# Kernel tuning notes

Hardware: AMD Instinct MI355X
Metric: run time of the kernel (lower is better)

## Reference

```python
import jax, jax.numpy as jnp
import numpy as np

B, S, D, H = 2, 2048, 1024, 16
DH = D // H  # head_dim = 64


def setup_inputs() -> dict:
    key = jax.random.key(0)
    ks = jax.random.split(key, 10)
    inp = {
        "query": jax.random.normal(ks[0], (B, S, D), jnp.float32),
        "key": jax.random.normal(ks[1], (B, S, D), jnp.float32),
        "value": jax.random.normal(ks[2], (B, S, D), jnp.float32),
        "mask": jnp.ones((B, S), jnp.int32),
        # per-head q/k/v projections stacked over the head axis [H, D, DH]
        "Wq": jax.random.normal(ks[3], (H, D, DH), jnp.float32) * 0.02,
        "bq": jnp.zeros((H, DH), jnp.float32),
        "Wk": jax.random.normal(ks[4], (H, D, DH), jnp.float32) * 0.02,
        "bk": jnp.zeros((H, DH), jnp.float32),
        "Wv": jax.random.normal(ks[5], (H, D, DH), jnp.float32) * 0.02,
        "bv": jnp.zeros((H, DH), jnp.float32),
        # output projection fc: Linear(D, D)
        "Wo": jax.random.normal(ks[6], (D, D), jnp.float32) * 0.02,
        "bo": jnp.zeros((D,), jnp.float32),
    }
    return inp


def reference(query, key, value, mask, Wq, bq, Wk, bk, Wv, bv, Wo, bo):
    scale = 1.0 / jnp.sqrt(jnp.asarray(DH, query.dtype))
    # batched per-head projections: [B,S,D] x [H,D,DH] -> [B,H,S,DH]
    q = jnp.einsum('bsd,hde->bhse', query, Wq) + bq[None, :, None, :]
    k = jnp.einsum('bsd,hde->bhse', key, Wk) + bk[None, :, None, :]
    v = jnp.einsum('bsd,hde->bhse', value, Wv) + bv[None, :, None, :]
    # scaled dot-product attention scores [B,H,Sq,Sk]
    scores = jnp.einsum('bhqe,bhke->bhqk', q, k) * scale
    scores = jnp.where(mask[:, None, None, :] == 0, jnp.asarray(-1e9, scores.dtype), scores)
    attn = jax.nn.softmax(scores, axis=-1)
    ctx = jnp.einsum('bhqk,bhke->bhqe', attn, v)          # [B,H,S,DH]
    ctx = ctx.transpose(0, 2, 1, 3).reshape(query.shape[0], -1, H * DH)  # concat heads
    return ctx @ Wo + bo
```

## Files before the change

kernel.cpp:

```cpp
#include <hip/hip_runtime.h>
#include <stdint.h>
#include <math.h>


typedef __attribute__((ext_vector_type(8))) short short8;
typedef __attribute__((ext_vector_type(4))) float floatx4;

#define LOG2E 1.44269504088896340736f

__device__ __forceinline__ unsigned short f32_bf16(float f) {
  union { float f; unsigned u; } c; c.f = f;
  return (unsigned short)((c.u + 0x7FFFu + ((c.u >> 16) & 1u)) >> 16);
}
__device__ __forceinline__ float bf16_f32(unsigned short u) {
  union { unsigned u; float f; } c; c.u = ((unsigned)u) << 16;
  return c.f;
}
__device__ __forceinline__ void gld16(const void* g, void* l) {
  __builtin_amdgcn_global_load_lds((const __attribute__((address_space(1))) void*)g,
                                   (__attribute__((address_space(3))) void*)l, 16, 0, 0);
}


__global__ __launch_bounds__(256) void prep_kernel(
    const float* __restrict__ qf, const float* __restrict__ kf, const float* __restrict__ vf,
    const float* __restrict__ w0, const float* __restrict__ w1, const float* __restrict__ w2,
    const float* __restrict__ wo, const int* __restrict__ mask,
    unsigned short* __restrict__ oq, unsigned short* __restrict__ ok, unsigned short* __restrict__ ov,
    unsigned short* __restrict__ o0, unsigned short* __restrict__ o1, unsigned short* __restrict__ o2,
    unsigned short* __restrict__ oo, float* __restrict__ mb) {
  __shared__ float t[32][33];
  const int y = blockIdx.y, bx = blockIdx.x;
  if (y < 3) {
    if (y == 0 && bx < 16) {
      int j = bx * 256 + threadIdx.x;
      mb[j] = (mask[j] == 0) ? (-1.0e9f * LOG2E) : 0.0f;
    }
    const float* in = (y == 0) ? qf : (y == 1) ? kf : vf;
    unsigned short* out = (y == 0) ? oq : (y == 1) ? ok : ov;
    int i = bx * 256 + threadIdx.x;
    float4 v = reinterpret_cast<const float4*>(in)[i];
    ushort4 o;
    o.x = f32_bf16(v.x); o.y = f32_bf16(v.y); o.z = f32_bf16(v.z); o.w = f32_bf16(v.w);
    reinterpret_cast<ushort4*>(out)[i] = o;
    return;
  }
  const int tx = threadIdx.x & 31, ty = threadIdx.x >> 5;
  const float* in; unsigned short* out; int R, C, z, r0, c0;
  if (bx < 3072) {
    const int zb = bx >> 6, rem = bx & 63;
    const int sel = zb >> 4; z = zb & 15;
    in = (sel == 0) ? w0 : (sel == 1) ? w1 : w2;
    out = (sel == 0) ? o0 : (sel == 1) ? o1 : o2;
    R = 1024; C = 64; r0 = (rem >> 1) * 32; c0 = (rem & 1) * 32;
  } else {
    const int t2 = bx - 3072;
    in = wo; out = oo; R = 1024; C = 1024; z = 0;
    r0 = (t2 >> 5) * 32; c0 = (t2 & 31) * 32;
  }
  const float* inp = in + (size_t)z * R * C;
  #pragma unroll
  for (int j = 0; j < 4; ++j)
    t[ty + j * 8][tx] = inp[(size_t)(r0 + ty + j * 8) * C + c0 + tx];
  __syncthreads();
  #pragma unroll
  for (int j = 0; j < 4; ++j)
    out[((size_t)z * C + c0 + ty + j * 8) * R + r0 + tx] = f32_bf16(t[tx][ty + j * 8]);
}


__global__ __launch_bounds__(512, 2) void gemm_proj_kernel(
    const unsigned short* __restrict__ qin, const unsigned short* __restrict__ kin,
    const unsigned short* __restrict__ vin,
    const unsigned short* __restrict__ WqT, const unsigned short* __restrict__ WkT,
    const unsigned short* __restrict__ WvT,
    const float* __restrict__ bq, const float* __restrict__ bk, const float* __restrict__ bv,
    unsigned short* __restrict__ Qp, unsigned short* __restrict__ Kp,
    unsigned short* __restrict__ Vt) {
  __shared__ unsigned short As[2][2][128 * 64];
  __shared__ unsigned short Bs[2][2][128 * 64];

  const int z = blockIdx.y;
  const int x = blockIdx.x;
  const int r = x & 7, q = x >> 3;
  int mt, nt;
  if (z < 2) { mt = r * 2 + (q >> 2); nt = q & 3; }
  else       { nt = r * 2 + (q >> 2); mt = q & 3; }
  const int blockM = mt * 256, blockN = nt * 256;

  const unsigned short* A  = (z == 0) ? qin : (z == 1) ? kin : WvT;
  const unsigned short* Bt = (z == 0) ? WqT : (z == 1) ? WkT : vin;
  const float* bias = (z == 0) ? bq : (z == 1) ? bk : bv;

  const int tid = threadIdx.x;
  const int w = tid >> 6, lane = tid & 63;
  const int quad = lane >> 4, l15 = lane & 15;
  const int wm = w & 1, wn = w >> 1;

  const int lr8 = lane >> 3;
  const int lc8 = lane & 7;
  const int gcs = lc8 ^ lr8;

  auto stage = [&](int k0, int buf) {
    #pragma unroll
    for (int h = 0; h < 2; ++h)
      #pragma unroll
      for (int s2 = 0; s2 < 2; ++s2) {
        const int rl = s2 * 64 + w * 8;
        gld16(A + (size_t)(blockM + h * 128 + rl + lr8) * 1024 + k0 + gcs * 8,
              &As[buf][h][rl * 64]);
      }
    #pragma unroll
    for (int h = 0; h < 2; ++h)
      #pragma unroll
      for (int s2 = 0; s2 < 2; ++s2) {
        const int rl = s2 * 64 + w * 8;
        gld16(Bt + (size_t)(blockN + h * 128 + rl + lr8) * 1024 + k0 + gcs * 8,
              &Bs[buf][h][rl * 64]);
      }
  };

  floatx4 acc[8][4];
  #pragma unroll
  for (int mi = 0; mi < 8; ++mi)
    #pragma unroll
    for (int ni = 0; ni < 4; ++ni)
      acc[mi][ni] = (floatx4){0.f, 0.f, 0.f, 0.f};

  stage(0, 0);
  __syncthreads();

  const int brb = (wn & 1) * 64;

  for (int st = 0; st < 16; ++st) {
    const int buf = st & 1;
    const unsigned short* Ah = &As[buf][wm][0];
    const unsigned short* Bh = &Bs[buf][wn >> 1][0];
    short8 af[4][2], b0[2][2], b1[2][2];

    if (st + 1 < 16) stage((st + 1) * 64, buf ^ 1);
    #pragma unroll
    for (int mi = 0; mi < 4; ++mi) {
      const int row = mi * 16 + l15;
      #pragma unroll
      for (int kk = 0; kk < 2; ++kk)
        af[mi][kk] = *(const short8*)(Ah + row * 64 + (((kk * 4 + quad) ^ (row & 7)) << 3));
    }
    #pragma unroll
    for (int ni = 0; ni < 2; ++ni) {
      const int row = brb + ni * 16 + l15;
      #pragma unroll
      for (int kk = 0; kk < 2; ++kk)
        b0[ni][kk] = *(const short8*)(Bh + row * 64 + (((kk * 4 + quad) ^ (row & 7)) << 3));
    }
    __builtin_amdgcn_s_barrier();
    __builtin_amdgcn_s_setprio(1);
    #pragma unroll
    for (int mi = 0; mi < 4; ++mi)
      #pragma unroll
      for (int ni = 0; ni < 2; ++ni)
        #pragma unroll
        for (int kk = 0; kk < 2; ++kk)
          acc[mi][ni] = __builtin_amdgcn_mfma_f32_16x16x32_bf16(af[mi][kk], b0[ni][kk], acc[mi][ni], 0, 0, 0);
    __builtin_amdgcn_s_setprio(0);
    __builtin_amdgcn_s_barrier();

    #pragma unroll
    for (int ni = 0; ni < 2; ++ni) {
      const int row = brb + (ni + 2) * 16 + l15;
      #pragma unroll
      for (int kk = 0; kk < 2; ++kk)
        b1[ni][kk] = *(const short8*)(Bh + row * 64 + (((kk * 4 + quad) ^ (row & 7)) << 3));
    }
    __builtin_amdgcn_s_barrier();
    __builtin_amdgcn_s_setprio(1);
    #pragma unroll
    for (int mi = 0; mi < 4; ++mi)
      #pragma unroll
      for (int ni = 0; ni < 2; ++ni)
        #pragma unroll
        for (int kk = 0; kk < 2; ++kk)
          acc[mi][ni + 2] = __builtin_amdgcn_mfma_f32_16x16x32_bf16(af[mi][kk], b1[ni][kk], acc[mi][ni + 2], 0, 0, 0);
    __builtin_amdgcn_s_setprio(0);
    __builtin_amdgcn_s_barrier();

    #pragma unroll
    for (int mi = 0; mi < 4; ++mi) {
      const int row = (mi + 4) * 16 + l15;
      #pragma unroll
      for (int kk = 0; kk < 2; ++kk)
        af[mi][kk] = *(const short8*)(Ah + row * 64 + (((kk * 4 + quad) ^ (row & 7)) << 3));
    }
    __builtin_amdgcn_s_barrier();
    __builtin_amdgcn_s_setprio(1);
    #pragma unroll
    for (int mi = 0; mi < 4; ++mi)
      #pragma unroll
      for (int ni = 0; ni < 2; ++ni)
        #pragma unroll
        for (int kk = 0; kk < 2; ++kk)
          acc[mi + 4][ni + 2] = __builtin_amdgcn_mfma_f32_16x16x32_bf16(af[mi][kk], b1[ni][kk], acc[mi + 4][ni + 2], 0, 0, 0);
    __builtin_amdgcn_s_setprio(0);
    __builtin_amdgcn_s_barrier();

    __builtin_amdgcn_s_setprio(1);
    #pragma unroll
    for (int mi = 0; mi < 4; ++mi)
      #pragma unroll
      for (int ni = 0; ni < 2; ++ni)
        #pragma unroll
        for (int kk = 0; kk < 2; ++kk)
          acc[mi + 4][ni] = __builtin_amdgcn_mfma_f32_16x16x32_bf16(af[mi][kk], b0[ni][kk], acc[mi + 4][ni], 0, 0, 0);
    __builtin_amdgcn_s_setprio(0);
    __syncthreads();
  }

  unsigned short* Cw = (w < 4) ? ((unsigned short*)As + w * 8192)
                               : ((unsigned short*)Bs + (w - 4) * 8192);
  const int pc = lc8 ^ lr8;

  if (z < 2) {
    unsigned short* outp = z ? Kp : Qp;
    const int n0 = blockN + wn * 64;
    const int m0 = blockM + wm * 128;
    float bn[4];
    #pragma unroll
    for (int ni = 0; ni < 4; ++ni) bn[ni] = bias[n0 + ni * 16 + l15];
    #pragma unroll
    for (int mi = 0; mi < 8; ++mi)
      #pragma unroll
      for (int ni = 0; ni < 4; ++ni)
        #pragma unroll
        for (int rr = 0; rr < 4; ++rr) {
          const int row = mi * 16 + quad * 4 + rr;
          const int col = ni * 16 + l15;
          Cw[row * 64 + (((col >> 3) ^ (row & 7)) << 3) + (col & 7)] =
              f32_bf16(acc[mi][ni][rr] + bn[ni]);
        }
    const size_t bb = (size_t)(m0 >> 11);
    const int h = n0 >> 6, s0 = m0 & 2047;
    unsigned short* dst = outp + ((bb * 16 + h) * 2048 + s0) * 64;
    #pragma unroll
    for (int ps = 0; ps < 16; ++ps) {
      const int lr = ps * 8 + lr8;
      *(short8*)(dst + lr * 64 + lc8 * 8) = *(const short8*)(Cw + lr * 64 + pc * 8);
    }
  } else {
    const int m0 = blockM + wm * 128;
    const int n0 = blockN + wn * 64;
    #pragma unroll
    for (int mi = 0; mi < 8; ++mi) {
      float bm[4];
      #pragma unroll
      for (int rr = 0; rr < 4; ++rr) bm[rr] = bias[m0 + mi * 16 + quad * 4 + rr];
      #pragma unroll
      for (int ni = 0; ni < 4; ++ni)
        #pragma unroll
        for (int rr = 0; rr < 4; ++rr) {
          const int row = mi * 16 + quad * 4 + rr;
          const int col = ni * 16 + l15;
          Cw[row * 64 + (((col >> 3) ^ (row & 7)) << 3) + (col & 7)] =
              f32_bf16(acc[mi][ni][rr] + bm[rr]);
        }
    }
    const size_t bb = (size_t)(n0 >> 11);
    const int s0 = n0 & 2047;
    unsigned short* dst = Vt + (bb * 1024 + m0) * 2048 + s0;
    #pragma unroll
    for (int ps = 0; ps < 16; ++ps) {
      const int lr = ps * 8 + lr8;
      *(short8*)(dst + (size_t)lr * 2048 + lc8 * 8) = *(const short8*)(Cw + lr * 64 + pc * 8);
    }
  }
}


__global__ __launch_bounds__(256) void gemm_out_kernel(
    const unsigned short* __restrict__ A, const unsigned short* __restrict__ Bt,
    const float* __restrict__ bias, float* __restrict__ out, int K, int N) {
  __shared__ unsigned short As[2][128 * 64];
  __shared__ unsigned short Bs[2][64 * 64];
  const int tid = threadIdx.x;
  const int w = tid >> 6, lane = tid & 63;
  const int quad = lane >> 4, l15 = lane & 15;
  const int wm = w & 1, wn = w >> 1;
  const int lr8 = lane >> 3, lc8 = lane & 7;
  const int gcs = lc8 ^ lr8;
  const int l = blockIdx.x, r = l & 7, j = l >> 3;
  const int blockM = (r * 4 + (j & 3)) * 128;
  const int blockN = (j >> 2) * 64;

  floatx4 acc[4][2];
  #pragma unroll
  for (int mi = 0; mi < 4; ++mi)
    #pragma unroll
    for (int ni = 0; ni < 2; ++ni)
      acc[mi][ni] = (floatx4){0.f, 0.f, 0.f, 0.f};

  auto stage = [&](int k0, int buf) {
    #pragma unroll
    for (int i = 0; i < 4; ++i) {
      const int rl = w * 32 + i * 8;
      gld16(A + (size_t)(blockM + rl + lr8) * K + k0 + gcs * 8, As[buf] + rl * 64);
    }
    #pragma unroll
    for (int i = 0; i < 2; ++i) {
      const int rl = w * 16 + i * 8;
      gld16(Bt + (size_t)(blockN + rl + lr8) * K + k0 + gcs * 8, Bs[buf] + rl * 64);
    }
  };

  const int iters = K >> 6;
  stage(0, 0);
  for (int it = 0; it < iters; ++it) {
    __syncthreads();
    if (it + 1 < iters) stage((it + 1) * 64, (it + 1) & 1);
    const unsigned short* Asb = As[it & 1];
    const unsigned short* Bsb = Bs[it & 1];
    short8 bf[2][2];
    #pragma unroll
    for (int ni = 0; ni < 2; ++ni) {
      const int row = wn * 32 + ni * 16 + l15;
      #pragma unroll
      for (int kk = 0; kk < 2; ++kk)
        bf[ni][kk] = *(const short8*)(Bsb + row * 64 + (((kk * 4 + quad) ^ (row & 7)) << 3));
    }
    #pragma unroll
    for (int mi = 0; mi < 4; ++mi) {
      const int row = wm * 64 + mi * 16 + l15;
      #pragma unroll
      for (int kk = 0; kk < 2; ++kk) {
        short8 af = *(const short8*)(Asb + row * 64 + (((kk * 4 + quad) ^ (row & 7)) << 3));
        #pragma unroll
        for (int ni = 0; ni < 2; ++ni)
          acc[mi][ni] = __builtin_amdgcn_mfma_f32_16x16x32_bf16(af, bf[ni][kk], acc[mi][ni], 0, 0, 0);
      }
    }
  }

  #pragma unroll
  for (int mi = 0; mi < 4; ++mi)
    #pragma unroll
    for (int ni = 0; ni < 2; ++ni) {
      const int n = blockN + wn * 32 + ni * 16 + l15;
      const float bv = bias[n];
      #pragma unroll
      for (int rr = 0; rr < 4; ++rr) {
        const int m = blockM + wm * 64 + mi * 16 + quad * 4 + rr;
        out[(size_t)m * N + n] = acc[mi][ni][rr] + bv;
      }
    }
}


__global__ __launch_bounds__(256) void attn_kernel(
    const unsigned short* __restrict__ Q, const unsigned short* __restrict__ Kg,
    const unsigned short* __restrict__ Vt, const float* __restrict__ maskAdd,
    unsigned short* __restrict__ ctx) {
  const int S = 2048;
  const int tid = threadIdx.x;
  const int w = tid >> 6, lane = tid & 63, quad = lane >> 4, l15 = lane & 15;
  const int l = blockIdx.x, r8 = l & 7, j8 = l >> 3;
  const int bh = r8 * 4 + (j8 & 3);
  const int qb = j8 >> 2;
  const int b = bh >> 4, h = bh & 15;
  const int q0 = qb * 128;

  __shared__ unsigned short Ks[2][128 * 64];
  __shared__ unsigned short Vs[2][64 * 128];
  __shared__ unsigned short Ps[4][32 * 64];
  unsigned short* Pw = Ps[w];

  const unsigned short* Qb = Q + (size_t)bh * S * 64;
  const unsigned short* Kb = Kg + (size_t)bh * S * 64;
  const unsigned short* Vb = Vt + (size_t)bh * 64 * S;
  const float* mb = maskAdd + (size_t)b * S;

  const float qs = 0.125f * LOG2E;
  short8 qf[2][2];
  #pragma unroll
  for (int mi = 0; mi < 2; ++mi)
    #pragma unroll
    for (int kq = 0; kq < 2; ++kq) {
      short8 v = *(const short8*)(Qb + (size_t)(q0 + w * 32 + mi * 16 + l15) * 64 + kq * 32 + quad * 8);
      #pragma unroll
      for (int jj = 0; jj < 8; ++jj)
        v[jj] = (short)f32_bf16(bf16_f32((unsigned short)v[jj]) * qs);
      qf[mi][kq] = v;
    }

  short8 onesf;
  #pragma unroll
  for (int jj = 0; jj < 8; ++jj) onesf[jj] = (short)0x3F80;

  floatx4 O[2][4], ls[2];
  #pragma unroll
  for (int mi = 0; mi < 2; ++mi) {
    #pragma unroll
    for (int ne = 0; ne < 4; ++ne) O[mi][ne] = (floatx4){0.f, 0.f, 0.f, 0.f};
    ls[mi] = (floatx4){0.f, 0.f, 0.f, 0.f};
  }

  auto stage_kv = [&](int t, int buf) {
    const int kv0 = t * 128;
    #pragma unroll
    for (int i = 0; i < 4; ++i) {
      int r0 = w * 32 + i * 8;
      int row = r0 + (lane >> 3);
      int cg = (lane & 7) ^ (row & 7);
      gld16(Kb + (size_t)(kv0 + row) * 64 + cg * 8, Ks[buf] + r0 * 64);
    }
    #pragma unroll
    for (int i = 0; i < 4; ++i) {
      int r0 = w * 16 + i * 4;
      int row = r0 + (lane >> 4);
      int p = lane & 15;
      int cg = (p & 8) | ((p & 7) ^ (row & 7));
      gld16(Vb + (size_t)row * S + kv0 + cg * 8, Vs[buf] + r0 * 128);
    }
  };

  stage_kv(0, 0);
  for (int t = 0; t < 16; ++t) {
    const int kv0 = t * 128;
    __syncthreads();
    float ma[8];
    #pragma unroll
    for (int ni = 0; ni < 8; ++ni) ma[ni] = mb[kv0 + ni * 16 + l15];
    if (t + 1 < 16) stage_kv(t + 1, (t + 1) & 1);
    const unsigned short* Ksb = Ks[t & 1];
    const unsigned short* Vsb = Vs[t & 1];

    #pragma unroll
    for (int ph = 0; ph < 2; ++ph) {
      floatx4 sc[2][4];
      #pragma unroll
      for (int ni = 0; ni < 4; ++ni) {
        const int key = (ph * 4 + ni) * 16 + l15;
        short8 kf0 = *(const short8*)(Ksb + key * 64 + ((quad) ^ (l15 & 7)) * 8);
        short8 kf1 = *(const short8*)(Ksb + key * 64 + ((4 + quad) ^ (l15 & 7)) * 8);
        #pragma unroll
        for (int mi = 0; mi < 2; ++mi) {
          floatx4 s = (floatx4){0.f, 0.f, 0.f, 0.f};
          s = __builtin_amdgcn_mfma_f32_16x16x32_bf16(qf[mi][0], kf0, s, 0, 0, 0);
          s = __builtin_amdgcn_mfma_f32_16x16x32_bf16(qf[mi][1], kf1, s, 0, 0, 0);
          sc[mi][ni] = s;
        }
      }
      #pragma unroll
      for (int mi = 0; mi < 2; ++mi)
        #pragma unroll
        for (int rr = 0; rr < 4; ++rr) {
          const int row = mi * 16 + quad * 4 + rr;
          const int g = (row + (row >> 3)) & 7;
          #pragma unroll
          for (int ni = 0; ni < 4; ++ni) {
            float p = __builtin_amdgcn_exp2f(sc[mi][ni][rr] + ma[ph * 4 + ni]);
            union { float f; unsigned u; } c; c.f = p;
            const int ch = (ni * 2 + (l15 >> 3)) ^ g;
            Pw[row * 64 + (ch & 7) * 8 + (l15 & 7)] = (unsigned short)(c.u >> 16);
          }
        }
      #pragma unroll
      for (int kkl = 0; kkl < 2; ++kkl) {
        const int kk = ph * 2 + kkl;
        short8 pfr[2], vfr[4];
        #pragma unroll
        for (int mi = 0; mi < 2; ++mi) {
          const int gp = (2 * mi + l15 + (l15 >> 3)) & 7;
          pfr[mi] = *(const short8*)(Pw + (mi * 16 + l15) * 64 + ((kkl * 4 + quad) ^ gp) * 8);
        }
        #pragma unroll
        for (int ne = 0; ne < 4; ++ne) {
          const int c = kk * 4 + quad;
          vfr[ne] = *(const short8*)(Vsb + (ne * 16 + l15) * 128 + ((c & 8) | ((c & 7) ^ (l15 & 7))) * 8);
        }
        #pragma unroll
        for (int mi = 0; mi < 2; ++mi) {
          #pragma unroll
          for (int ne = 0; ne < 4; ++ne)
            O[mi][ne] = __builtin_amdgcn_mfma_f32_16x16x32_bf16(pfr[mi], vfr[ne], O[mi][ne], 0, 0, 0);
          ls[mi] = __builtin_amdgcn_mfma_f32_16x16x32_bf16(pfr[mi], onesf, ls[mi], 0, 0, 0);
        }
      }
    }
  }

  #pragma unroll
  for (int mi = 0; mi < 2; ++mi)
    #pragma unroll
    for (int rr = 0; rr < 4; ++rr) {
      const float inv = __builtin_amdgcn_rcpf(ls[mi][rr]);
      const int s = q0 + w * 32 + mi * 16 + quad * 4 + rr;
      #pragma unroll
      for (int ne = 0; ne < 4; ++ne)
        ctx[((size_t)b * S + s) * 1024 + h * 64 + ne * 16 + l15] = f32_bf16(O[mi][ne][rr] * inv);
    }
}


extern "C" void kernel_launch(void* const* d_in, const int* in_sizes, int n_in,
                              void* d_out, int out_size, void* d_ws, size_t ws_size,
                              hipStream_t stream) {
  const float* query = (const float*)d_in[0];
  const float* key   = (const float*)d_in[1];
  const float* value = (const float*)d_in[2];
  const int*   mask  = (const int*)d_in[3];
  const float* Wq = (const float*)d_in[4];
  const float* bq = (const float*)d_in[5];
  const float* Wk = (const float*)d_in[6];
  const float* bk = (const float*)d_in[7];
  const float* Wv = (const float*)d_in[8];
  const float* bv = (const float*)d_in[9];
  const float* Wo = (const float*)d_in[10];
  const float* bo = (const float*)d_in[11];
  float* out = (float*)d_out;

  char* ws = (char*)d_ws;
  const size_t MB = 1024 * 1024;
  unsigned short* qin  = (unsigned short*)(ws + 0);
  unsigned short* kin  = (unsigned short*)(ws + 8 * MB);
  unsigned short* vin  = (unsigned short*)(ws + 16 * MB);
  unsigned short* WqT  = (unsigned short*)(ws + 24 * MB);
  unsigned short* WkT  = (unsigned short*)(ws + 26 * MB);
  unsigned short* WvT  = (unsigned short*)(ws + 28 * MB);
  unsigned short* WoT  = (unsigned short*)(ws + 30 * MB);
  unsigned short* Qp   = (unsigned short*)(ws + 32 * MB);
  unsigned short* Kp   = (unsigned short*)(ws + 40 * MB);
  unsigned short* Vt   = (unsigned short*)(ws + 48 * MB);
  float* maskAdd       = (float*)(ws + 56 * MB);
  unsigned short* ctxb = qin;

  prep_kernel<<<dim3(4096, 4), 256, 0, stream>>>(query, key, value, Wq, Wk, Wv, Wo, mask,
                                                 qin, kin, vin, WqT, WkT, WvT, WoT, maskAdd);
  gemm_proj_kernel<<<dim3(64, 3), 512, 0, stream>>>(qin, kin, vin, WqT, WkT, WvT,
                                                    bq, bk, bv, Qp, Kp, Vt);
  attn_kernel<<<dim3(512), 256, 0, stream>>>(Qp, Kp, Vt, maskAdd, ctxb);
  gemm_out_kernel<<<dim3(512), 256, 0, stream>>>(ctxb, WoT, bo, out, 1024, 1024);
}
```

Baseline: 229.4 us.

## Shrink projection GEMM tiles to 128x128 with 256 threads and simpler pipeline

The QKV projection GEMM moves from 256x256 tiles with 512 threads to 128x128 tiles with 256 threads, so the grid grows from 192 to 768 blocks. This is meant to fill the GPU's compute units better, since 192 blocks underfill a 256-CU device. The interleaved barrier and setprio MFMA schedule is replaced with a plain double-buffered loop. In exchange each block reuses less data per load, raising global and LDS traffic per FLOP, and loses the fine-grained load/compute interleaving.

```diff
diff --git a/kernel.cpp b/kernel.cpp
--- a/kernel.cpp
+++ b/kernel.cpp
@@ -69,7 +69,7 @@
 }
 
 
-__global__ __launch_bounds__(512, 2) void gemm_proj_kernel(
+__global__ __launch_bounds__(256) void gemm_proj_kernel(
     const unsigned short* __restrict__ qin, const unsigned short* __restrict__ kin,
     const unsigned short* __restrict__ vin,
     const unsigned short* __restrict__ WqT, const unsigned short* __restrict__ WkT,
@@ -77,16 +77,15 @@
     const float* __restrict__ bq, const float* __restrict__ bk, const float* __restrict__ bv,
     unsigned short* __restrict__ Qp, unsigned short* __restrict__ Kp,
     unsigned short* __restrict__ Vt) {
-  __shared__ unsigned short As[2][2][128 * 64];
-  __shared__ unsigned short Bs[2][2][128 * 64];
-
-  const int z = blockIdx.y;
-  const int x = blockIdx.x;
-  const int r = x & 7, q = x >> 3;
+  __shared__ unsigned short As[2][128 * 64];
+  __shared__ unsigned short Bs[2][128 * 64];
+
+  const int z = blockIdx.y, bx = blockIdx.x;
+  const int r = bx & 7, j = bx >> 3;
   int mt, nt;
-  if (z < 2) { mt = r * 2 + (q >> 2); nt = q & 3; }
-  else       { nt = r * 2 + (q >> 2); mt = q & 3; }
-  const int blockM = mt * 256, blockN = nt * 256;
+  if (z < 2) { mt = r * 4 + (j & 3); nt = j >> 2; }
+  else       { nt = r * 4 + (j & 3); mt = j >> 2; }
+  const int blockM = mt * 128, blockN = nt * 128;
 
   const unsigned short* A  = (z == 0) ? qin : (z == 1) ? kin : WvT;
   const unsigned short* Bt = (z == 0) ? WqT : (z == 1) ? WkT : vin;
@@ -96,138 +95,69 @@
   const int w = tid >> 6, lane = tid & 63;
   const int quad = lane >> 4, l15 = lane & 15;
   const int wm = w & 1, wn = w >> 1;
-
-  const int lr8 = lane >> 3;
-  const int lc8 = lane & 7;
+  const int lr8 = lane >> 3, lc8 = lane & 7;
   const int gcs = lc8 ^ lr8;
 
   auto stage = [&](int k0, int buf) {
     #pragma unroll
-    for (int h = 0; h < 2; ++h)
-      #pragma unroll
-      for (int s2 = 0; s2 < 2; ++s2) {
-        const int rl = s2 * 64 + w * 8;
-        gld16(A + (size_t)(blockM + h * 128 + rl + lr8) * 1024 + k0 + gcs * 8,
-              &As[buf][h][rl * 64]);
-      }
-    #pragma unroll
-    for (int h = 0; h < 2; ++h)
-      #pragma unroll
-      for (int s2 = 0; s2 < 2; ++s2) {
-        const int rl = s2 * 64 + w * 8;
-        gld16(Bt + (size_t)(blockN + h * 128 + rl + lr8) * 1024 + k0 + gcs * 8,
-              &Bs[buf][h][rl * 64]);
-      }
+    for (int i = 0; i < 4; ++i) {
+      const int rl = w * 32 + i * 8;
+      gld16(A + (size_t)(blockM + rl + lr8) * 1024 + k0 + gcs * 8, As[buf] + rl * 64);
+    }
+    #pragma unroll
+    for (int i = 0; i < 4; ++i) {
+      const int rl = w * 32 + i * 8;
+      gld16(Bt + (size_t)(blockN + rl + lr8) * 1024 + k0 + gcs * 8, Bs[buf] + rl * 64);
+    }
   };
 
-  floatx4 acc[8][4];
-  #pragma unroll
-  for (int mi = 0; mi < 8; ++mi)
+  floatx4 acc[4][4];
+  #pragma unroll
+  for (int mi = 0; mi < 4; ++mi)
     #pragma unroll
     for (int ni = 0; ni < 4; ++ni)
       acc[mi][ni] = (floatx4){0.f, 0.f, 0.f, 0.f};
 
   stage(0, 0);
+  for (int it = 0; it < 16; ++it) {
+    __syncthreads();
+    if (it + 1 < 16) stage((it + 1) * 64, (it + 1) & 1);
+    const unsigned short* Asb = As[it & 1];
+    const unsigned short* Bsb = Bs[it & 1];
+    short8 bf[4][2];
+    #pragma unroll
+    for (int ni = 0; ni < 4; ++ni) {
+      const int row = wn * 64 + ni * 16 + l15;
+      #pragma unroll
+      for (int kk = 0; kk < 2; ++kk)
+        bf[ni][kk] = *(const short8*)(Bsb + row * 64 + (((kk * 4 + quad) ^ (row & 7)) << 3));
+    }
+    #pragma unroll
+    for (int mi = 0; mi < 4; ++mi) {
+      const int row = wm * 64 + mi * 16 + l15;
+      #pragma unroll
+      for (int kk = 0; kk < 2; ++kk) {
+        short8 af = *(const short8*)(Asb + row * 64 + (((kk * 4 + quad) ^ (row & 7)) << 3));
+        #pragma unroll
+        for (int ni = 0; ni < 4; ++ni)
+          acc[mi][ni] = __builtin_amdgcn_mfma_f32_16x16x32_bf16(af, bf[ni][kk], acc[mi][ni], 0, 0, 0);
+      }
+    }
+  }
   __syncthreads();
 
-  const int brb = (wn & 1) * 64;
-
-  for (int st = 0; st < 16; ++st) {
-    const int buf = st & 1;
-    const unsigned short* Ah = &As[buf][wm][0];
-    const unsigned short* Bh = &Bs[buf][wn >> 1][0];
-    short8 af[4][2], b0[2][2], b1[2][2];
-
-    if (st + 1 < 16) stage((st + 1) * 64, buf ^ 1);
-    #pragma unroll
-    for (int mi = 0; mi < 4; ++mi) {
-      const int row = mi * 16 + l15;
-      #pragma unroll
-      for (int kk = 0; kk < 2; ++kk)
-        af[mi][kk] = *(const short8*)(Ah + row * 64 + (((kk * 4 + quad) ^ (row & 7)) << 3));
-    }
-    #pragma unroll
-    for (int ni = 0; ni < 2; ++ni) {
-      const int row = brb + ni * 16 + l15;
-      #pragma unroll
-      for (int kk = 0; kk < 2; ++kk)
-        b0[ni][kk] = *(const short8*)(Bh + row * 64 + (((kk * 4 + quad) ^ (row & 7)) << 3));
-    }
-    __builtin_amdgcn_s_barrier();
-    __builtin_amdgcn_s_setprio(1);
-    #pragma unroll
-    for (int mi = 0; mi < 4; ++mi)
-      #pragma unroll
-      for (int ni = 0; ni < 2; ++ni)
-        #pragma unroll
-        for (int kk = 0; kk < 2; ++kk)
-          acc[mi][ni] = __builtin_amdgcn_mfma_f32_16x16x32_bf16(af[mi][kk], b0[ni][kk], acc[mi][ni], 0, 0, 0);
-    __builtin_amdgcn_s_setprio(0);
-    __builtin_amdgcn_s_barrier();
-
-    #pragma unroll
-    for (int ni = 0; ni < 2; ++ni) {
-      const int row = brb + (ni + 2) * 16 + l15;
-      #pragma unroll
-      for (int kk = 0; kk < 2; ++kk)
-        b1[ni][kk] = *(const short8*)(Bh + row * 64 + (((kk * 4 + quad) ^ (row & 7)) << 3));
-    }
-    __builtin_amdgcn_s_barrier();
-    __builtin_amdgcn_s_setprio(1);
-    #pragma unroll
-    for (int mi = 0; mi < 4; ++mi)
-      #pragma unroll
-      for (int ni = 0; ni < 2; ++ni)
-        #pragma unroll
-        for (int kk = 0; kk < 2; ++kk)
-          acc[mi][ni + 2] = __builtin_amdgcn_mfma_f32_16x16x32_bf16(af[mi][kk], b1[ni][kk], acc[mi][ni + 2], 0, 0, 0);
-    __builtin_amdgcn_s_setprio(0);
-    __builtin_amdgcn_s_barrier();
-
-    #pragma unroll
-    for (int mi = 0; mi < 4; ++mi) {
-      const int row = (mi + 4) * 16 + l15;
-      #pragma unroll
-      for (int kk = 0; kk < 2; ++kk)
-        af[mi][kk] = *(const short8*)(Ah + row * 64 + (((kk * 4 + quad) ^ (row & 7)) << 3));
-    }
-    __builtin_amdgcn_s_barrier();
-    __builtin_amdgcn_s_setprio(1);
-    #pragma unroll
-    for (int mi = 0; mi < 4; ++mi)
-      #pragma unroll
-      for (int ni = 0; ni < 2; ++ni)
-        #pragma unroll
-        for (int kk = 0; kk < 2; ++kk)
-          acc[mi + 4][ni + 2] = __builtin_amdgcn_mfma_f32_16x16x32_bf16(af[mi][kk], b1[ni][kk], acc[mi + 4][ni + 2], 0, 0, 0);
-    __builtin_amdgcn_s_setprio(0);
-    __builtin_amdgcn_s_barrier();
-
-    __builtin_amdgcn_s_setprio(1);
-    #pragma unroll
-    for (int mi = 0; mi < 4; ++mi)
-      #pragma unroll
-      for (int ni = 0; ni < 2; ++ni)
-        #pragma unroll
-        for (int kk = 0; kk < 2; ++kk)
-          acc[mi + 4][ni] = __builtin_amdgcn_mfma_f32_16x16x32_bf16(af[mi][kk], b0[ni][kk], acc[mi + 4][ni], 0, 0, 0);
-    __builtin_amdgcn_s_setprio(0);
-    __syncthreads();
-  }
-
-  unsigned short* Cw = (w < 4) ? ((unsigned short*)As + w * 8192)
-                               : ((unsigned short*)Bs + (w - 4) * 8192);
+  unsigned short* Cw = (unsigned short*)As + w * 4096;
   const int pc = lc8 ^ lr8;
 
   if (z < 2) {
     unsigned short* outp = z ? Kp : Qp;
     const int n0 = blockN + wn * 64;
-    const int m0 = blockM + wm * 128;
+    const int m0 = blockM + wm * 64;
     float bn[4];
     #pragma unroll
     for (int ni = 0; ni < 4; ++ni) bn[ni] = bias[n0 + ni * 16 + l15];
     #pragma unroll
-    for (int mi = 0; mi < 8; ++mi)
+    for (int mi = 0; mi < 4; ++mi)
       #pragma unroll
       for (int ni = 0; ni < 4; ++ni)
         #pragma unroll
@@ -241,15 +171,15 @@
     const int h = n0 >> 6, s0 = m0 & 2047;
     unsigned short* dst = outp + ((bb * 16 + h) * 2048 + s0) * 64;
     #pragma unroll
-    for (int ps = 0; ps < 16; ++ps) {
+    for (int ps = 0; ps < 8; ++ps) {
       const int lr = ps * 8 + lr8;
       *(short8*)(dst + lr * 64 + lc8 * 8) = *(const short8*)(Cw + lr * 64 + pc * 8);
     }
   } else {
-    const int m0 = blockM + wm * 128;
+    const int m0 = blockM + wm * 64;
     const int n0 = blockN + wn * 64;
     #pragma unroll
-    for (int mi = 0; mi < 8; ++mi) {
+    for (int mi = 0; mi < 4; ++mi) {
       float bm[4];
       #pragma unroll
       for (int rr = 0; rr < 4; ++rr) bm[rr] = bias[m0 + mi * 16 + quad * 4 + rr];
@@ -267,7 +197,7 @@
     const int s0 = n0 & 2047;
     unsigned short* dst = Vt + (bb * 1024 + m0) * 2048 + s0;
     #pragma unroll
-    for (int ps = 0; ps < 16; ++ps) {
+    for (int ps = 0; ps < 8; ++ps) {
       const int lr = ps * 8 + lr8;
       *(short8*)(dst + (size_t)lr * 2048 + lc8 * 8) = *(const short8*)(Cw + lr * 64 + pc * 8);
     }
@@ -533,8 +463,8 @@
 
   prep_kernel<<<dim3(4096, 4), 256, 0, stream>>>(query, key, value, Wq, Wk, Wv, Wo, mask,
                                                  qin, kin, vin, WqT, WkT, WvT, WoT, maskAdd);
-  gemm_proj_kernel<<<dim3(64, 3), 512, 0, stream>>>(qin, kin, vin, WqT, WkT, WvT,
-                                                    bq, bk, bv, Qp, Kp, Vt);
+  gemm_proj_kernel<<<dim3(256, 3), 256, 0, stream>>>(qin, kin, vin, WqT, WkT, WvT,
+                                                     bq, bk, bv, Qp, Kp, Vt);
   attn_kernel<<<dim3(512), 256, 0, stream>>>(Qp, Kp, Vt, maskAdd, ctxb);
   gemm_out_kernel<<<dim3(512), 256, 0, stream>>>(ctxb, WoT, bo, out, 1024, 1024);
 }
```

New measurement: 237.1 us. 1.03x slower.
